# Kernel optimization log

Hardware: AMD Instinct MI355X
Metric: run time of the kernel (lower is better)

The kernel has to match this reference:

```python
import jax, jax.numpy as jnp
import numpy as np

D = 64        # inner_feature_len (dim)
HID = 128     # hidden_channels of the edge MLP
NCONV = 2     # n_conv
STEPS = 3     # Set2Set processing_steps
NSEG = 128    # number of graphs in the batch


def setup_inputs() -> dict:
    key = jax.random.key(0)
    ks = jax.random.split(key, 30)
    N, E, FN, FE = 10000, 64000, 92, 41
    s = 0.05
    p = lambda i, shape: jax.random.normal(ks[i], shape, jnp.float32) * s
    return {
        "x": jax.random.normal(ks[0], (N, FN), jnp.float32),
        "edge_attr": jax.random.uniform(ks[1], (E, FE), dtype=jnp.float32),
        "lin0_w": p(2, (D, FN)), "lin0_b": p(3, (D,)),
        "nn1_w": p(4, (HID, FE)), "nn1_b": p(5, (HID,)),
        "nn2_w": p(6, (D * D, HID)), "nn2_b": p(7, (D * D,)),
        "root_w": p(8, (D, D)), "conv_b": p(9, (D,)),
        "gru_w_ih": p(10, (3 * D, D)), "gru_w_hh": p(11, (3 * D, D)),
        "gru_b_ih": p(12, (3 * D,)), "gru_b_hh": p(13, (3 * D,)),
        "lstm_w_ih": p(14, (4 * D, 2 * D)), "lstm_w_hh": p(15, (4 * D, D)),
        "lstm_b_ih": p(16, (4 * D,)), "lstm_b_hh": p(17, (4 * D,)),
        "lin1_w": p(18, (D, 2 * D)), "lin1_b": p(19, (D,)),
        "lin2_w": p(20, (1, D)), "lin2_b": p(21, (1,)),
        "edge_index": jax.random.randint(ks[22], (2, E), 0, N, dtype=jnp.int32),
        "batch": jnp.sort(jax.random.randint(ks[23], (N,), 0, NSEG, dtype=jnp.int32)),
    }


def _gru_step(m, h, w_ih, w_hh, b_ih, b_hh):
    # torch GRU gate order: r, z, n
    gi = m @ w_ih.T + b_ih
    gh = h @ w_hh.T + b_hh
    r = jax.nn.sigmoid(gi[:, :D] + gh[:, :D])
    z = jax.nn.sigmoid(gi[:, D:2 * D] + gh[:, D:2 * D])
    n = jnp.tanh(gi[:, 2 * D:] + r * gh[:, 2 * D:])
    return (1.0 - z) * n + z * h


def _forward(x, edge_attr, lin0_w, lin0_b, nn1_w, nn1_b, nn2_w, nn2_b, root_w, conv_b,
             gru_w_ih, gru_w_hh, gru_b_ih, gru_b_hh, lstm_w_ih, lstm_w_hh, lstm_b_ih,
             lstm_b_hh, lin1_w, lin1_b, lin2_w, lin2_b, edge_index, batch):
    N = x.shape[0]
    src, dst = edge_index[0], edge_index[1]

    # Edge-conditioned weight matrices: [E, D, D] (dominant intermediate)
    We = (jax.nn.relu(edge_attr @ nn1_w.T + nn1_b) @ nn2_w.T + nn2_b).reshape(-1, D, D)
    deg = jnp.clip(jax.ops.segment_sum(jnp.ones_like(src, jnp.float32), dst, num_segments=N), 1.0, None)

    out = jax.nn.relu(x @ lin0_w.T + lin0_b)   # [N, D]
    h = out                                     # GRU hidden (num_layers=1)
    for _ in range(NCONV):
        # NNConv: gather -> per-edge matmul -> scatter-mean, plus root transform + bias
        msg = jnp.einsum('ei,eio->eo', out[src], We)                 # [E, D]
        agg = jax.ops.segment_sum(msg, dst, num_segments=N) / deg[:, None]
        m = jax.nn.relu(agg + out @ root_w.T + conv_b)
        h = _gru_step(m, h, gru_w_ih, gru_w_hh, gru_b_ih, gru_b_hh)
        out = h

    # Set2Set pooling (LSTM-attention readout)
    q_star = jnp.zeros((NSEG, 2 * D), x.dtype)
    hl = jnp.zeros((NSEG, D), x.dtype)
    cl = jnp.zeros((NSEG, D), x.dtype)
    for _ in range(STEPS):
        g = q_star @ lstm_w_ih.T + lstm_b_ih + hl @ lstm_w_hh.T + lstm_b_hh
        i = jax.nn.sigmoid(g[:, :D])
        f = jax.nn.sigmoid(g[:, D:2 * D])
        gg = jnp.tanh(g[:, 2 * D:3 * D])
        o = jax.nn.sigmoid(g[:, 3 * D:])
        cl = f * cl + i * gg
        hl = o * jnp.tanh(cl)
        q = hl                                   # [NSEG, D]
        e = jnp.sum(out * q[batch], axis=-1)     # [N]
        mmax = jax.ops.segment_max(e, batch, num_segments=NSEG)
        a = jnp.exp(e - mmax[batch])
        denom = jax.ops.segment_sum(a, batch, num_segments=NSEG)
        a = a / denom[batch]
        r = jax.ops.segment_sum(a[:, None] * out, batch, num_segments=NSEG)  # [NSEG, D]
        q_star = jnp.concatenate([q, r], axis=1)

    y = jax.nn.relu(q_star @ lin1_w.T + lin1_b) @ lin2_w.T + lin2_b
    return y.reshape(-1)


def reference(x, edge_attr, lin0_w, lin0_b, nn1_w, nn1_b, nn2_w, nn2_b, root_w, conv_b,
              gru_w_ih, gru_w_hh, gru_b_ih, gru_b_hh, lstm_w_ih, lstm_w_hh, lstm_b_ih,
              lstm_b_hh, lin1_w, lin1_b, lin2_w, lin2_b, edge_index, batch):
    return _forward(x, edge_attr, lin0_w, lin0_b, nn1_w, nn1_b, nn2_w, nn2_b, root_w,
                    conv_b, gru_w_ih, gru_w_hh, gru_b_ih, gru_b_hh, lstm_w_ih, lstm_w_hh,
                    lstm_b_ih, lstm_b_hh, lin1_w, lin1_b, lin2_w, lin2_b, edge_index, batch)
```

## Files before the change

### kernel.cpp

```cpp
#include <hip/hip_runtime.h>
#include <hip/hip_bf16.h>
#include <math.h>

#define DD 64
#define HIDC 128
#define FN 92
#define FE 41
#define S2CAP 192

typedef unsigned short u16;
typedef short bf16x8 __attribute__((ext_vector_type(8)));
typedef float f32x4 __attribute__((ext_vector_type(4)));

__device__ __forceinline__ float sigmoidf_(float x){ return 1.f/(1.f+expf(-x)); }

__device__ __forceinline__ u16 f2bf(float v){
  union { float f; unsigned u; } x; x.f = v;
  unsigned r = x.u + 0x7fff + ((x.u >> 16) & 1);
  return (u16)(r >> 16);
}
__device__ __forceinline__ float bf2f(u16 v){
  union { float f; unsigned u; } x; x.u = ((unsigned)v) << 16;
  return x.f;
}
__device__ __forceinline__ void split_bf(float v, u16& h, u16& l){
  h = f2bf(v); l = f2bf(v - bf2f(h));
}

__global__ void k_pack(const float* __restrict__ lin0_w, const float* __restrict__ nn1_w,
                       const float* __restrict__ root_w, const float* __restrict__ gwih,
                       const float* __restrict__ gwhh, const float* __restrict__ lwih,
                       const float* __restrict__ lwhh, const float* __restrict__ lin1_w,
                       float* __restrict__ lin0T, float* __restrict__ nn1T,
                       float* __restrict__ rootT, float* __restrict__ wihT,
                       float* __restrict__ whhT, float* __restrict__ lwihT,
                       float* __restrict__ lwhhT, float* __restrict__ lin1T)
{
  int idx = blockIdx.x*blockDim.x + threadIdx.x;
  if (idx < 92*64){ int k=idx/64, o=idx%64; lin0T[k*64+o] = lin0_w[o*92+k]; return; } idx -= 92*64;
  if (idx < 41*128){ int k=idx/128, h=idx%128; nn1T[k*128+h] = nn1_w[h*41+k]; return; } idx -= 41*128;
  if (idx < 64*64){ int i=idx/64, o=idx%64; rootT[i*64+o] = root_w[o*64+i]; return; } idx -= 64*64;
  if (idx < 64*192){ int i=idx/192, g=idx%192; wihT[i*192+g] = gwih[g*64+i]; return; } idx -= 64*192;
  if (idx < 64*192){ int i=idx/192, g=idx%192; whhT[i*192+g] = gwhh[g*64+i]; return; } idx -= 64*192;
  if (idx < 128*256){ int j=idx/256, t=idx%256; lwihT[j*256+t] = lwih[t*128+j]; return; } idx -= 128*256;
  if (idx < 64*256){ int j=idx/256, t=idx%256; lwhhT[j*256+t] = lwhh[t*64+j]; return; } idx -= 64*256;
  if (idx < 128*64){ int j=idx/64, t=idx%64; lin1T[j*64+t] = lin1_w[t*128+j]; return; }
}

__global__ void k_pack_b2(const float* __restrict__ nn2_w,
                          u16* __restrict__ BhT, u16* __restrict__ BlT){
  int idx = blockIdx.x*256 + threadIdx.x;
  if (idx >= 524288) return;
  int i  = idx & 63;
  int ho = (idx >> 6) & 4095;
  int c  = idx >> 18;
  int h = ho >> 6, o = ho & 63;
  float v = nn2_w[(size_t)(i*64+o)*128 + c*64 + h];
  u16 hi, lo; split_bf(v, hi, lo);
  BhT[idx] = hi; BlT[idx] = lo;
}

__global__ void k_pack_b1(const float* __restrict__ nn1_w,
                          u16* __restrict__ BT1h, u16* __restrict__ BT1l){
  int idx = blockIdx.x*256 + threadIdx.x;
  if (idx >= 8192) return;
  int h = idx >> 6, k = idx & 63;
  float v = (k < FE) ? nn1_w[(size_t)h*FE + k] : 0.f;
  u16 hi, lo; split_bf(v, hi, lo);
  BT1h[idx] = hi; BT1l[idx] = lo;
}

__global__ void k_split_ea(const float* __restrict__ ea, const int* __restrict__ sortedE,
                           u16* __restrict__ eaH, u16* __restrict__ eaL, int E){
  int idx = blockIdx.x*256 + threadIdx.x;
  if (idx >= E*64) return;
  int ew = idx >> 6, k = idx & 63;
  int e = sortedE[ew];
  float v = (k < FE) ? ea[(size_t)e*FE + k] : 0.f;
  u16 hi, lo; split_bf(v, hi, lo);
  eaH[idx] = hi; eaL[idx] = lo;
}

__global__ __launch_bounds__(256) void k_node_mlp(const float* __restrict__ x,
    const float* __restrict__ lin0T, const float* __restrict__ lin0_b,
    const float* __restrict__ nn2_b,
    float* __restrict__ out, u16* __restrict__ outH, u16* __restrict__ outL,
    float* __restrict__ bterm, int N)
{
  __shared__ float xs[4][FN];
  int base = blockIdx.x*4;
  for (int i=threadIdx.x; i<4*FN; i+=256){
    int n = base + i/FN;
    xs[i/FN][i%FN] = (n<N) ? x[(size_t)n*FN + i%FN] : 0.f;
  }
  __syncthreads();
  int ln = threadIdx.x>>6, o = threadIdx.x&63;
  int n = base+ln;
  if (n>=N) return;
  float acc = lin0_b[o];
  #pragma unroll 4
  for (int k=0;k<FN;k++) acc = fmaf(xs[ln][k], lin0T[k*64+o], acc);
  float v = fmaxf(acc, 0.f);
  out[(size_t)n*64+o] = v;
  u16 hi, lo; split_bf(v, hi, lo);
  outH[(size_t)n*64+o] = hi;
  outL[(size_t)n*64+o] = lo;
  float bt = 0.f;
  #pragma unroll 8
  for (int i=0;i<64;i++) bt = fmaf(__shfl(v, i, 64), nn2_b[i*64+o], bt);
  bterm[(size_t)n*64+o] = bt;
}

__global__ void k_count(const int* __restrict__ dst, const int* __restrict__ src,
                        float* __restrict__ deg, int* __restrict__ scnt, int E){
  int e = blockIdx.x*blockDim.x + threadIdx.x;
  if (e < E){
    atomicAdd(&deg[dst[e]], 1.f);
    atomicAdd(&scnt[src[e]], 1);
  }
}

__global__ void k_scan1(const int* __restrict__ cnt, int* __restrict__ excl,
                        int* __restrict__ bsum, int N){
  __shared__ int buf[256];
  int i = blockIdx.x*256 + threadIdx.x;
  int v = (i<N) ? cnt[i] : 0;
  buf[threadIdx.x] = v;
  __syncthreads();
  #pragma unroll
  for (int off=1; off<256; off<<=1){
    int t = (threadIdx.x>=off) ? buf[threadIdx.x-off] : 0;
    __syncthreads();
    buf[threadIdx.x] += t;
    __syncthreads();
  }
  if (i<N) excl[i] = buf[threadIdx.x] - v;
  if (threadIdx.x==255) bsum[blockIdx.x] = buf[255];
}
__global__ void k_scan2(int* __restrict__ bsum, int nb){
  __shared__ int buf[256];
  int v = (threadIdx.x<nb) ? bsum[threadIdx.x] : 0;
  buf[threadIdx.x] = v;
  __syncthreads();
  #pragma unroll
  for (int off=1; off<256; off<<=1){
    int t = (threadIdx.x>=off) ? buf[threadIdx.x-off] : 0;
    __syncthreads();
    buf[threadIdx.x] += t;
    __syncthreads();
  }
  if (threadIdx.x<nb) bsum[threadIdx.x] = buf[threadIdx.x] - v;
}
__global__ void k_scan3(int* __restrict__ starts, int* __restrict__ cursor,
                        const int* __restrict__ bsum, int N, int E){
  int i = blockIdx.x*256 + threadIdx.x;
  if (i<N){
    int s = starts[i] + bsum[blockIdx.x];
    starts[i] = s;
    cursor[i] = s;
  }
  if (i==0) starts[N] = E;
}

__global__ void k_sort(const int* __restrict__ src, const int* __restrict__ dst,
                       int* __restrict__ cursor, int* __restrict__ sortedE,
                       int* __restrict__ srcS, int* __restrict__ dstS, int E){
  int e = blockIdx.x*256 + threadIdx.x;
  if (e < E){
    int s = src[e];
    int p = atomicAdd(&cursor[s], 1);
    sortedE[p] = e;
    srcS[p] = s;
    dstS[p] = dst[e];
  }
}

__global__ __launch_bounds__(256,3) void k_edge_mlp_mfma(
    const u16* __restrict__ eaH, const u16* __restrict__ eaL,
    const u16* __restrict__ BT1h, const u16* __restrict__ BT1l,
    const float* __restrict__ nn1_b, float* __restrict__ hidden, int E)
{
  __shared__ float st[4][16][68];
  const int wave = threadIdx.x >> 6;
  const int lane = threadIdx.x & 63;
  const int row  = lane & 15;
  const int quad = lane >> 4;
  const int m0 = blockIdx.x*128 + (wave>>1)*64;
  const int n0 = (wave&1)*64;

  bf16x8 AH0[4], AH1[4], AL0[4], AL1[4];
  #pragma unroll
  for (int p=0;p<4;p++){
    int ar = min(m0 + p*16 + row, E-1);
    const u16* aH = eaH + (size_t)ar*64 + quad*8;
    const u16* aL = eaL + (size_t)ar*64 + quad*8;
    AH0[p] = *(const bf16x8*)(aH);
    AH1[p] = *(const bf16x8*)(aH + 32);
    AL0[p] = *(const bf16x8*)(aL);
    AL1[p] = *(const bf16x8*)(aL + 32);
  }
  f32x4 acc[4][4];
  #pragma unroll
  for (int p=0;p<4;p++)
    #pragma unroll
    for (int t=0;t<4;t++) acc[p][t] = (f32x4){0.f,0.f,0.f,0.f};

  #pragma unroll
  for (int t=0;t<4;t++){
    const u16* bH = BT1h + (size_t)(n0 + t*16 + row)*64 + quad*8;
    const u16* bL = BT1l + (size_t)(n0 + t*16 + row)*64 + quad*8;
    bf16x8 bh0 = *(const bf16x8*)(bH);
    bf16x8 bh1 = *(const bf16x8*)(bH + 32);
    bf16x8 bl0 = *(const bf16x8*)(bL);
    bf16x8 bl1 = *(const bf16x8*)(bL + 32);
    #pragma unroll
    for (int p=0;p<4;p++){
      f32x4 a = acc[p][t];
      a = __builtin_amdgcn_mfma_f32_16x16x32_bf16(AH0[p], bh0, a, 0,0,0);
      a = __builtin_amdgcn_mfma_f32_16x16x32_bf16(AH1[p], bh1, a, 0,0,0);
      a = __builtin_amdgcn_mfma_f32_16x16x32_bf16(AH0[p], bl0, a, 0,0,0);
      a = __builtin_amdgcn_mfma_f32_16x16x32_bf16(AH1[p], bl1, a, 0,0,0);
      a = __builtin_amdgcn_mfma_f32_16x16x32_bf16(AL0[p], bh0, a, 0,0,0);
      a = __builtin_amdgcn_mfma_f32_16x16x32_bf16(AL1[p], bh1, a, 0,0,0);
      acc[p][t] = a;
    }
  }

  const int lr = lane >> 4;
  const int lc = (lane & 15) * 4;
  #pragma unroll
  for (int p=0;p<4;p++){
    #pragma unroll
    for (int t=0;t<4;t++){
      float bias = nn1_b[n0 + t*16 + row];
      #pragma unroll
      for (int r=0;r<4;r++) st[wave][quad*4+r][t*16+row] = fmaxf(acc[p][t][r] + bias, 0.f);
    }
    #pragma unroll
    for (int it=0; it<4; it++){
      int mrow = it*4 + lr;
      float4 v;
      v.x = st[wave][mrow][lc+0];
      v.y = st[wave][mrow][lc+1];
      v.z = st[wave][mrow][lc+2];
      v.w = st[wave][mrow][lc+3];
      int m = m0 + p*16 + mrow;
      if (m < E) *(float4*)(hidden + (size_t)m*128 + n0 + lc) = v;
    }
  }
}

__global__ __launch_bounds__(256,3) void k_qgemm_mfma(
    const u16* __restrict__ Ah, const u16* __restrict__ Al,
    const u16* __restrict__ BhT, const u16* __restrict__ BlT,
    float* __restrict__ C, int M)
{
  __shared__ float st[4][16][68];
  const int wave = threadIdx.x >> 6;
  const int lane = threadIdx.x & 63;
  const int row  = lane & 15;
  const int quad = lane >> 4;
  const int m0 = blockIdx.y * 64;
  const int n0 = blockIdx.x * 256 + wave * 64;

  bf16x8 AH0[4], AH1[4], AL0[4], AL1[4];
  #pragma unroll
  for (int p=0;p<4;p++){
    int ar = min(m0 + p*16 + row, M-1);
    const u16* aH = Ah + (size_t)ar*64 + quad*8;
    const u16* aL = Al + (size_t)ar*64 + quad*8;
    AH0[p] = *(const bf16x8*)(aH);
    AH1[p] = *(const bf16x8*)(aH + 32);
    AL0[p] = *(const bf16x8*)(aL);
    AL1[p] = *(const bf16x8*)(aL + 32);
  }
  f32x4 acc[4][4];
  #pragma unroll
  for (int p=0;p<4;p++)
    #pragma unroll
    for (int t=0;t<4;t++) acc[p][t] = (f32x4){0.f,0.f,0.f,0.f};

  #pragma unroll
  for (int t=0;t<4;t++){
    const u16* bH = BhT + (size_t)(n0 + t*16 + row)*64 + quad*8;
    const u16* bL = BlT + (size_t)(n0 + t*16 + row)*64 + quad*8;
    bf16x8 bh0 = *(const bf16x8*)(bH);
    bf16x8 bh1 = *(const bf16x8*)(bH + 32);
    bf16x8 bl0 = *(const bf16x8*)(bL);
    bf16x8 bl1 = *(const bf16x8*)(bL + 32);
    #pragma unroll
    for (int p=0;p<4;p++){
      f32x4 a = acc[p][t];
      a = __builtin_amdgcn_mfma_f32_16x16x32_bf16(AH0[p], bh0, a, 0,0,0);
      a = __builtin_amdgcn_mfma_f32_16x16x32_bf16(AH1[p], bh1, a, 0,0,0);
      a = __builtin_amdgcn_mfma_f32_16x16x32_bf16(AH0[p], bl0, a, 0,0,0);
      a = __builtin_amdgcn_mfma_f32_16x16x32_bf16(AH1[p], bl1, a, 0,0,0);
      a = __builtin_amdgcn_mfma_f32_16x16x32_bf16(AL0[p], bh0, a, 0,0,0);
      a = __builtin_amdgcn_mfma_f32_16x16x32_bf16(AL1[p], bh1, a, 0,0,0);
      acc[p][t] = a;
    }
  }

  const int lr = lane >> 4;
  const int lc = (lane & 15) * 4;
  #pragma unroll
  for (int p=0;p<4;p++){
    #pragma unroll
    for (int t=0;t<4;t++)
      #pragma unroll
      for (int r=0;r<4;r++) st[wave][quad*4+r][t*16+row] = acc[p][t][r];
    #pragma unroll
    for (int it=0; it<4; it++){
      int mrow = it*4 + lr;
      float4 v;
      v.x = st[wave][mrow][lc+0];
      v.y = st[wave][mrow][lc+1];
      v.z = st[wave][mrow][lc+2];
      v.w = st[wave][mrow][lc+3];
      int m = m0 + p*16 + mrow;
      if (m < M) *(float4*)(C + (size_t)m*4096 + n0 + lc) = v;
    }
  }
}

template<int PASS>
__global__ __launch_bounds__(256) void k_edge_gather(const float* __restrict__ Q,
    const float* __restrict__ hidden, int h0,
    const float* __restrict__ bterm, const int* __restrict__ srcS,
    const int* __restrict__ dstS,
    float* __restrict__ msg, float* __restrict__ agg, int E)
{
  __shared__ float hs[4][2][64];
  __shared__ float red[4][2][64];
  const int wv = threadIdx.x>>6, lane = threadIdx.x&63;
  const int ew0 = (blockIdx.x*4 + wv)*2;
  const bool v0 = (ew0 < E), v1 = (ew0+1 < E);
  const int e0 = v0 ? ew0 : 0;
  const int e1 = v1 ? ew0+1 : 0;
  const int s0 = srcS[e0], s1 = srcS[e1];
  hs[wv][0][lane] = hidden[(size_t)e0*128 + h0 + lane];
  hs[wv][1][lane] = hidden[(size_t)e1*128 + h0 + lane];
  const int sg = lane>>4, oq = lane&15;
  const float* q0 = Q + (size_t)s0*4096 + sg*64 + oq*4;
  const float* q1 = Q + (size_t)s1*4096 + sg*64 + oq*4;
  float a00=0.f,a01=0.f,a02=0.f,a03=0.f;
  float a10=0.f,a11=0.f,a12=0.f,a13=0.f;
  #pragma unroll
  for (int j=0;j<16;j++){
    float4 qa = *(const float4*)(q0 + j*256);
    float4 qb = *(const float4*)(q1 + j*256);
    float h0v = hs[wv][0][j*4 + sg];
    float h1v = hs[wv][1][j*4 + sg];
    a00 = fmaf(h0v, qa.x, a00); a01 = fmaf(h0v, qa.y, a01);
    a02 = fmaf(h0v, qa.z, a02); a03 = fmaf(h0v, qa.w, a03);
    a10 = fmaf(h1v, qb.x, a10); a11 = fmaf(h1v, qb.y, a11);
    a12 = fmaf(h1v, qb.z, a12); a13 = fmaf(h1v, qb.w, a13);
  }
  a00 += __shfl_xor(a00,16); a00 += __shfl_xor(a00,32);
  a01 += __shfl_xor(a01,16); a01 += __shfl_xor(a01,32);
  a02 += __shfl_xor(a02,16); a02 += __shfl_xor(a02,32);
  a03 += __shfl_xor(a03,16); a03 += __shfl_xor(a03,32);
  a10 += __shfl_xor(a10,16); a10 += __shfl_xor(a10,32);
  a11 += __shfl_xor(a11,16); a11 += __shfl_xor(a11,32);
  a12 += __shfl_xor(a12,16); a12 += __shfl_xor(a12,32);
  a13 += __shfl_xor(a13,16); a13 += __shfl_xor(a13,32);
  if (lane < 16){
    float4 r0; r0.x=a00; r0.y=a01; r0.z=a02; r0.w=a03;
    float4 r1; r1.x=a10; r1.y=a11; r1.z=a12; r1.w=a13;
    *(float4*)&red[wv][0][lane*4] = r0;
    *(float4*)&red[wv][1][lane*4] = r1;
  }
  if (v0){
    float rv = red[wv][0][lane];
    if (PASS == 0) msg[(size_t)ew0*64 + lane] = bterm[(size_t)s0*64 + lane] + rv;
    else atomicAdd(&agg[(size_t)dstS[ew0]*64 + lane], msg[(size_t)ew0*64 + lane] + rv);
  }
  if (v1){
    float rv = red[wv][1][lane];
    if (PASS == 0) msg[(size_t)(ew0+1)*64 + lane] = bterm[(size_t)s1*64 + lane] + rv;
    else atomicAdd(&agg[(size_t)dstS[ew0+1]*64 + lane], msg[(size_t)(ew0+1)*64 + lane] + rv);
  }
}

__global__ __launch_bounds__(256) void k_node_update(const float* __restrict__ outOld,
    const float* __restrict__ agg, const float* __restrict__ deg,
    const float* __restrict__ rootT, const float* __restrict__ conv_b,
    const float* __restrict__ wihT, const float* __restrict__ whhT,
    const float* __restrict__ b_ih, const float* __restrict__ b_hh,
    const float* __restrict__ nn2_b,
    float* __restrict__ outNew, u16* __restrict__ outH, u16* __restrict__ outL,
    float* __restrict__ bterm, int N)
{
  __shared__ float hs[4][64];
  __shared__ float ms[4][64];
  int ln = threadIdx.x>>6, o = threadIdx.x&63;
  int n = blockIdx.x*4+ln;
  bool ok = (n<N);
  float h = ok ? outOld[(size_t)n*64+o] : 0.f;
  hs[ln][o] = h;
  __syncthreads();
  float root = 0.f;
  #pragma unroll 8
  for (int i=0;i<64;i++) root = fmaf(hs[ln][i], rootT[i*64+o], root);
  float d = ok ? fmaxf(deg[n], 1.f) : 1.f;
  float a = ok ? agg[(size_t)n*64+o]/d : 0.f;
  float m = fmaxf(a + root + conv_b[o], 0.f);
  ms[ln][o] = m;
  __syncthreads();
  float gir=b_ih[o], giz=b_ih[64+o], gin=b_ih[128+o];
  float ghr=b_hh[o], ghz=b_hh[64+o], ghn=b_hh[128+o];
  #pragma unroll 4
  for (int i=0;i<64;i++){
    float mi = ms[ln][i], hi = hs[ln][i];
    gir = fmaf(mi, wihT[i*192+o],      gir);
    giz = fmaf(mi, wihT[i*192+64+o],   giz);
    gin = fmaf(mi, wihT[i*192+128+o],  gin);
    ghr = fmaf(hi, whhT[i*192+o],      ghr);
    ghz = fmaf(hi, whhT[i*192+64+o],   ghz);
    ghn = fmaf(hi, whhT[i*192+128+o],  ghn);
  }
  float r = sigmoidf_(gir+ghr);
  float z = sigmoidf_(giz+ghz);
  float nn = tanhf(gin + r*ghn);
  if (ok){
    float v = (1.f-z)*nn + z*h;
    outNew[(size_t)n*64+o] = v;
    u16 hi16, lo16; split_bf(v, hi16, lo16);
    outH[(size_t)n*64+o] = hi16;
    outL[(size_t)n*64+o] = lo16;
    float bt = 0.f;
    #pragma unroll 8
    for (int i=0;i<64;i++) bt = fmaf(__shfl(v, i, 64), nn2_b[i*64+o], bt);
    bterm[(size_t)n*64+o] = bt;
  }
}

__global__ __launch_bounds__(256) void k_set2set(const float* __restrict__ out,
    const int* __restrict__ batch, int N,
    const float* __restrict__ lwihT, const float* __restrict__ lwhhT,
    const float* __restrict__ b_ih, const float* __restrict__ b_hh,
    const float* __restrict__ lin1T, const float* __restrict__ lin1_b,
    const float* __restrict__ lin2_w, const float* __restrict__ lin2_b,
    float* __restrict__ y)
{
  __shared__ float X[S2CAP][65];
  __shared__ float earr[S2CAP];
  __shared__ float qstar[128], hl[64], cl[64], g[256];
  __shared__ float rpart[4][64], spart[4], redm[4], zs[64];
  __shared__ int sb[2];
  const int tid = threadIdx.x;
  const int b = blockIdx.x;
  const int wid = tid>>6, lane = tid&63;
  if (tid < 128) qstar[tid] = 0.f;
  if (tid < 64){ hl[tid]=0.f; cl[tid]=0.f; }
  if (tid == 0){
    int lo=0, hi=N;
    while (lo<hi){ int mid=(lo+hi)>>1; if (batch[mid] < b) lo=mid+1; else hi=mid; }
    sb[0]=lo;
    int lo2=lo, hi2=N;
    while (lo2<hi2){ int mid=(lo2+hi2)>>1; if (batch[mid] < b+1) lo2=mid+1; else hi2=mid; }
    sb[1]=lo2;
  }
  __syncthreads();
  const int nlo = sb[0], nhi = sb[1], nn = nhi - nlo;
  const bool single = (nn <= S2CAP);
  if (single){
    for (int idx = tid; idx < nn*64; idx += 256){
      X[idx>>6][idx&63] = out[(size_t)(nlo + (idx>>6))*64 + (idx&63)];
    }
  }
  __syncthreads();

  for (int step=0; step<3; step++){
    float gs = b_ih[tid] + b_hh[tid];
    for (int j=0;j<128;j++) gs = fmaf(qstar[j], lwihT[j*256+tid], gs);
    for (int j=0;j<64;j++)  gs = fmaf(hl[j],    lwhhT[j*256+tid], gs);
    g[tid] = gs;
    __syncthreads();
    if (tid < 64){
      float ig = sigmoidf_(g[tid]);
      float fg = sigmoidf_(g[64+tid]);
      float gg = tanhf(g[128+tid]);
      float og = sigmoidf_(g[192+tid]);
      float c = fg*cl[tid] + ig*gg;
      cl[tid] = c;
      hl[tid] = og*tanhf(c);
    }
    __syncthreads();

    if (single){
      float lm = -INFINITY;
      for (int n = tid; n < nn; n += 256){
        float acc = 0.f;
        #pragma unroll 8
        for (int d=0; d<64; d++) acc = fmaf(X[n][d], hl[d], acc);
        earr[n] = acc;
        lm = fmaxf(lm, acc);
      }
      lm = fmaxf(lm, __shfl_xor(lm,1));  lm = fmaxf(lm, __shfl_xor(lm,2));
      lm = fmaxf(lm, __shfl_xor(lm,4));  lm = fmaxf(lm, __shfl_xor(lm,8));
      lm = fmaxf(lm, __shfl_xor(lm,16)); lm = fmaxf(lm, __shfl_xor(lm,32));
      if (lane==0) redm[wid] = lm;
      __syncthreads();
      if (tid==0) redm[0] = fmaxf(fmaxf(redm[0],redm[1]), fmaxf(redm[2],redm[3]));
      __syncthreads();
      const float gmax = redm[0];
      float ls = 0.f;
      for (int n = tid; n < nn; n += 256){
        float a = expf(earr[n] - gmax);
        earr[n] = a;
        ls += a;
      }
      ls += __shfl_xor(ls,1);  ls += __shfl_xor(ls,2);  ls += __shfl_xor(ls,4);
      ls += __shfl_xor(ls,8);  ls += __shfl_xor(ls,16); ls += __shfl_xor(ls,32);
      if (lane==0) spart[wid] = ls;
      __syncthreads();
      float racc = 0.f;
      for (int n = wid; n < nn; n += 4) racc = fmaf(earr[n], X[n][lane], racc);
      rpart[wid][lane] = racc;
      __syncthreads();
      if (tid < 64){
        float r = rpart[0][tid]+rpart[1][tid]+rpart[2][tid]+rpart[3][tid];
        float s = spart[0]+spart[1]+spart[2]+spart[3];
        qstar[tid] = hl[tid];
        qstar[64+tid] = (nn>0) ? r/s : 0.f;
      }
      __syncthreads();
    } else {
      float qv = hl[lane];
      float lm = -INFINITY;
      for (int n = nlo + wid; n < nhi; n += 4){
        float p = out[(size_t)n*64 + lane]*qv;
        p += __shfl_xor(p,1); p += __shfl_xor(p,2); p += __shfl_xor(p,4);
        p += __shfl_xor(p,8); p += __shfl_xor(p,16); p += __shfl_xor(p,32);
        lm = fmaxf(lm, p);
      }
      if (lane==0) redm[wid] = lm;
      __syncthreads();
      if (tid==0) redm[0] = fmaxf(fmaxf(redm[0],redm[1]), fmaxf(redm[2],redm[3]));
      __syncthreads();
      float gmax = redm[0];
      float sw = 0.f, racc = 0.f;
      for (int n = nlo + wid; n < nhi; n += 4){
        float ol = out[(size_t)n*64 + lane];
        float p = ol*qv;
        p += __shfl_xor(p,1); p += __shfl_xor(p,2); p += __shfl_xor(p,4);
        p += __shfl_xor(p,8); p += __shfl_xor(p,16); p += __shfl_xor(p,32);
        float a = expf(p - gmax);
        sw += a;
        racc = fmaf(a, ol, racc);
      }
      rpart[wid][lane] = racc;
      if (lane==0) spart[wid] = sw;
      __syncthreads();
      if (tid < 64){
        float r = rpart[0][tid]+rpart[1][tid]+rpart[2][tid]+rpart[3][tid];
        float s = spart[0]+spart[1]+spart[2]+spart[3];
        qstar[tid] = hl[tid];
        qstar[64+tid] = (nn>0) ? r/s : 0.f;
      }
      __syncthreads();
    }
  }
  if (tid < 64){
    float acc = lin1_b[tid];
    for (int j=0;j<128;j++) acc = fmaf(qstar[j], lin1T[j*64+tid], acc);
    zs[tid] = fmaxf(acc, 0.f);
  }
  __syncthreads();
  if (tid < 64){
    float v = zs[lane]*lin2_w[lane];
    v += __shfl_xor(v,1); v += __shfl_xor(v,2); v += __shfl_xor(v,4);
    v += __shfl_xor(v,8); v += __shfl_xor(v,16); v += __shfl_xor(v,32);
    if (lane==0) y[b] = v + lin2_b[0];
  }
}

extern "C" void kernel_launch(void* const* d_in, const int* in_sizes, int n_in,
                              void* d_out, int out_size, void* d_ws, size_t ws_size,
                              hipStream_t stream)
{
  const float* x      = (const float*)d_in[0];
  const float* eattr  = (const float*)d_in[1];
  const float* lin0_w = (const float*)d_in[2];
  const float* lin0_b = (const float*)d_in[3];
  const float* nn1_w  = (const float*)d_in[4];
  const float* nn1_b  = (const float*)d_in[5];
  const float* nn2_w  = (const float*)d_in[6];
  const float* nn2_b  = (const float*)d_in[7];
  const float* root_w = (const float*)d_in[8];
  const float* conv_b = (const float*)d_in[9];
  const float* gwih   = (const float*)d_in[10];
  const float* gwhh   = (const float*)d_in[11];
  const float* gbih   = (const float*)d_in[12];
  const float* gbhh   = (const float*)d_in[13];
  const float* lwih   = (const float*)d_in[14];
  const float* lwhh   = (const float*)d_in[15];
  const float* lbih   = (const float*)d_in[16];
  const float* lbhh   = (const float*)d_in[17];
  const float* lin1_w = (const float*)d_in[18];
  const float* lin1_b = (const float*)d_in[19];
  const float* lin2_w = (const float*)d_in[20];
  const float* lin2_b = (const float*)d_in[21];
  const int*   eidx   = (const int*)d_in[22];
  const int*   batch  = (const int*)d_in[23];

  const int N = in_sizes[0]/FN;
  const int E = in_sizes[1]/FE;
  const int* srcI = eidx;
  const int* dstI = eidx + E;

  char* w = (char*)d_ws;
  size_t off = 0;
  auto alloc = [&](size_t bytes)->char* {
    char* p = w + off;
    off = (off + bytes + 255) & ~(size_t)255;
    return p;
  };
  float* degw  = (float*)alloc((size_t)N*4);
  int*   scnt  = (int*)alloc((size_t)N*4);
  int*   starts= (int*)alloc((size_t)(N+1)*4);
  int*   cursor= (int*)alloc((size_t)N*4);
  int*   bsum  = (int*)alloc((size_t)256*4);
  int*   sortedE=(int*)alloc((size_t)E*4);
  int*   srcS  = (int*)alloc((size_t)E*4);
  int*   dstS  = (int*)alloc((size_t)E*4);
  float* outA  = (float*)alloc((size_t)N*64*4);
  float* outB  = (float*)alloc((size_t)N*64*4);
  u16*   outAH = (u16*)alloc((size_t)N*64*2);
  u16*   outAL = (u16*)alloc((size_t)N*64*2);
  u16*   outBH = (u16*)alloc((size_t)N*64*2);
  u16*   outBL = (u16*)alloc((size_t)N*64*2);
  float* agg   = (float*)alloc((size_t)N*64*4);
  float* bterm = (float*)alloc((size_t)N*64*4);
  float* hidden= (float*)alloc((size_t)E*128*4);
  float* msg   = (float*)alloc((size_t)E*64*4);
  u16*   B2hT  = (u16*)alloc((size_t)524288*2);
  u16*   B2lT  = (u16*)alloc((size_t)524288*2);
  u16*   BT1h  = (u16*)alloc((size_t)8192*2);
  u16*   BT1l  = (u16*)alloc((size_t)8192*2);
  float* lin0T = (float*)alloc((size_t)92*64*4);
  float* nn1T  = (float*)alloc((size_t)41*128*4);
  float* rootT = (float*)alloc((size_t)64*64*4);
  float* wihT  = (float*)alloc((size_t)64*192*4);
  float* whhT  = (float*)alloc((size_t)64*192*4);
  float* lwihT = (float*)alloc((size_t)128*256*4);
  float* lwhhT = (float*)alloc((size_t)64*256*4);
  float* lin1T = (float*)alloc((size_t)128*64*4);
  float* Q     = (float*)alloc((size_t)N*4096*4);
  u16* eaH = (u16*)Q;
  u16* eaL = eaH + (size_t)E*64;

  const int NB = (N+255)/256;

  hipMemsetAsync(degw, 0, (size_t)N*4, stream);
  hipMemsetAsync(scnt, 0, (size_t)N*4, stream);
  k_pack<<<(97152+255)/256, 256, 0, stream>>>(lin0_w, nn1_w, root_w, gwih, gwhh,
      lwih, lwhh, lin1_w, lin0T, nn1T, rootT, wihT, whhT, lwihT, lwhhT, lin1T);
  k_pack_b2<<<524288/256, 256, 0, stream>>>(nn2_w, B2hT, B2lT);
  k_pack_b1<<<8192/256, 256, 0, stream>>>(nn1_w, BT1h, BT1l);
  k_node_mlp<<<(N+3)/4, 256, 0, stream>>>(x, lin0T, lin0_b, nn2_b, outA, outAH, outAL, bterm, N);
  k_count<<<(E+255)/256, 256, 0, stream>>>(dstI, srcI, degw, scnt, E);
  k_scan1<<<NB, 256, 0, stream>>>(scnt, starts, bsum, N);
  k_scan2<<<1, 256, 0, stream>>>(bsum, NB);
  k_scan3<<<NB, 256, 0, stream>>>(starts, cursor, bsum, N, E);
  k_sort<<<(E+255)/256, 256, 0, stream>>>(srcI, dstI, cursor, sortedE, srcS, dstS, E);
  k_split_ea<<<((size_t)E*64+255)/256, 256, 0, stream>>>(eattr, sortedE, eaH, eaL, E);
  k_edge_mlp_mfma<<<(E+127)/128, 256, 0, stream>>>(eaH, eaL, BT1h, BT1l, nn1_b, hidden, E);

  float* cur = outA; float* nxt = outB;
  u16* curH = outAH; u16* curL = outAL;
  u16* nxtH = outBH; u16* nxtL = outBL;
  const dim3 qgrid(16, (N+63)/64);
  const int gatherGx = (E+7)/8;
  for (int conv=0; conv<2; conv++){
    hipMemsetAsync(agg, 0, (size_t)N*64*4, stream);
    k_qgemm_mfma<<<qgrid, 256, 0, stream>>>(curH, curL, B2hT, B2lT, Q, N);
    k_edge_gather<0><<<gatherGx, 256, 0, stream>>>(Q, hidden, 0, bterm, srcS, dstS, msg, agg, E);
    k_qgemm_mfma<<<qgrid, 256, 0, stream>>>(curH, curL, B2hT + 262144, B2lT + 262144, Q, N);
    k_edge_gather<1><<<gatherGx, 256, 0, stream>>>(Q, hidden, 64, bterm, srcS, dstS, msg, agg, E);
    k_node_update<<<(N+3)/4, 256, 0, stream>>>(cur, agg, degw, rootT, conv_b,
        wihT, whhT, gbih, gbhh, nn2_b, nxt, nxtH, nxtL, bterm, N);
    float* t = cur; cur = nxt; nxt = t;
    u16* th = curH; curH = nxtH; nxtH = th;
    u16* tl = curL; curL = nxtL; nxtL = tl;
  }

  k_set2set<<<128, 256, 0, stream>>>(cur, batch, N, lwihT, lwhhT, lbih, lbhh,
      lin1T, lin1_b, lin2_w, lin2_b, (float*)d_out);
}
```

Measured before the change: 667.0 us.

## Swap MFMA operand order to store directly, and process four edges per wave in gather

The two MFMA GEMM kernels now pass the B tile as the first operand and the A tile as the second. Each lane then holds four consecutive output columns of one row, so results can be written as float4 straight to global memory. This drops the shared-memory staging buffer and the full accumulator array, which should cut LDS traffic and register pressure. Separately, the edge gather kernel handles four edges per wave instead of two, with the grid halved to match, to raise memory-level parallelism on the Q row loads at the cost of more registers.

```diff
diff --git a/kernel.cpp b/kernel.cpp
--- a/kernel.cpp
+++ b/kernel.cpp
@@ -180,9 +180,8 @@
     const u16* __restrict__ BT1h, const u16* __restrict__ BT1l,
     const float* __restrict__ nn1_b, float* __restrict__ hidden, int E)
 {
-  __shared__ float st[4][16][68];
+  const int lane = threadIdx.x & 63;
   const int wave = threadIdx.x >> 6;
-  const int lane = threadIdx.x & 63;
   const int row  = lane & 15;
   const int quad = lane >> 4;
   const int m0 = blockIdx.x*128 + (wave>>1)*64;
@@ -199,53 +198,36 @@
     AL0[p] = *(const bf16x8*)(aL);
     AL1[p] = *(const bf16x8*)(aL + 32);
   }
-  f32x4 acc[4][4];
-  #pragma unroll
-  for (int p=0;p<4;p++)
-    #pragma unroll
-    for (int t=0;t<4;t++) acc[p][t] = (f32x4){0.f,0.f,0.f,0.f};
-
-  #pragma unroll
-  for (int t=0;t<4;t++){
-    const u16* bH = BT1h + (size_t)(n0 + t*16 + row)*64 + quad*8;
-    const u16* bL = BT1l + (size_t)(n0 + t*16 + row)*64 + quad*8;
+  #pragma unroll
+  for (int tb=0;tb<4;tb++){
+    const u16* bH = BT1h + (size_t)(n0 + tb*16 + row)*64 + quad*8;
+    const u16* bL = BT1l + (size_t)(n0 + tb*16 + row)*64 + quad*8;
     bf16x8 bh0 = *(const bf16x8*)(bH);
     bf16x8 bh1 = *(const bf16x8*)(bH + 32);
     bf16x8 bl0 = *(const bf16x8*)(bL);
     bf16x8 bl1 = *(const bf16x8*)(bL + 32);
+    float4 bias;
+    {
+      int nb = n0 + tb*16 + quad*4;
+      bias.x = nn1_b[nb+0]; bias.y = nn1_b[nb+1];
+      bias.z = nn1_b[nb+2]; bias.w = nn1_b[nb+3];
+    }
     #pragma unroll
-    for (int p=0;p<4;p++){
-      f32x4 a = acc[p][t];
-      a = __builtin_amdgcn_mfma_f32_16x16x32_bf16(AH0[p], bh0, a, 0,0,0);
-      a = __builtin_amdgcn_mfma_f32_16x16x32_bf16(AH1[p], bh1, a, 0,0,0);
-      a = __builtin_amdgcn_mfma_f32_16x16x32_bf16(AH0[p], bl0, a, 0,0,0);
-      a = __builtin_amdgcn_mfma_f32_16x16x32_bf16(AH1[p], bl1, a, 0,0,0);
-      a = __builtin_amdgcn_mfma_f32_16x16x32_bf16(AL0[p], bh0, a, 0,0,0);
-      a = __builtin_amdgcn_mfma_f32_16x16x32_bf16(AL1[p], bh1, a, 0,0,0);
-      acc[p][t] = a;
-    }
-  }
-
-  const int lr = lane >> 4;
-  const int lc = (lane & 15) * 4;
-  #pragma unroll
-  for (int p=0;p<4;p++){
-    #pragma unroll
-    for (int t=0;t<4;t++){
-      float bias = nn1_b[n0 + t*16 + row];
-      #pragma unroll
-      for (int r=0;r<4;r++) st[wave][quad*4+r][t*16+row] = fmaxf(acc[p][t][r] + bias, 0.f);
-    }
-    #pragma unroll
-    for (int it=0; it<4; it++){
-      int mrow = it*4 + lr;
-      float4 v;
-      v.x = st[wave][mrow][lc+0];
-      v.y = st[wave][mrow][lc+1];
-      v.z = st[wave][mrow][lc+2];
-      v.w = st[wave][mrow][lc+3];
-      int m = m0 + p*16 + mrow;
-      if (m < E) *(float4*)(hidden + (size_t)m*128 + n0 + lc) = v;
+    for (int ta=0;ta<4;ta++){
+      f32x4 a = {0.f,0.f,0.f,0.f};
+      a = __builtin_amdgcn_mfma_f32_16x16x32_bf16(bh0, AH0[ta], a, 0,0,0);
+      a = __builtin_amdgcn_mfma_f32_16x16x32_bf16(bh1, AH1[ta], a, 0,0,0);
+      a = __builtin_amdgcn_mfma_f32_16x16x32_bf16(bl0, AH0[ta], a, 0,0,0);
+      a = __builtin_amdgcn_mfma_f32_16x16x32_bf16(bl1, AH1[ta], a, 0,0,0);
+      a = __builtin_amdgcn_mfma_f32_16x16x32_bf16(bh0, AL0[ta], a, 0,0,0);
+      a = __builtin_amdgcn_mfma_f32_16x16x32_bf16(bh1, AL1[ta], a, 0,0,0);
+      int m = m0 + ta*16 + row;
+      if (m < E){
+        float4 v;
+        v.x = fmaxf(a[0]+bias.x, 0.f); v.y = fmaxf(a[1]+bias.y, 0.f);
+        v.z = fmaxf(a[2]+bias.z, 0.f); v.w = fmaxf(a[3]+bias.w, 0.f);
+        *(float4*)(hidden + (size_t)m*128 + n0 + tb*16 + quad*4) = v;
+      }
     }
   }
 }
@@ -255,9 +237,8 @@
     const u16* __restrict__ BhT, const u16* __restrict__ BlT,
     float* __restrict__ C, int M)
 {
-  __shared__ float st[4][16][68];
+  const int lane = threadIdx.x & 63;
   const int wave = threadIdx.x >> 6;
-  const int lane = threadIdx.x & 63;
   const int row  = lane & 15;
   const int quad = lane >> 4;
   const int m0 = blockIdx.y * 64;
@@ -274,51 +255,29 @@
     AL0[p] = *(const bf16x8*)(aL);
     AL1[p] = *(const bf16x8*)(aL + 32);
   }
-  f32x4 acc[4][4];
-  #pragma unroll
-  for (int p=0;p<4;p++)
-    #pragma unroll
-    for (int t=0;t<4;t++) acc[p][t] = (f32x4){0.f,0.f,0.f,0.f};
-
-  #pragma unroll
-  for (int t=0;t<4;t++){
-    const u16* bH = BhT + (size_t)(n0 + t*16 + row)*64 + quad*8;
-    const u16* bL = BlT + (size_t)(n0 + t*16 + row)*64 + quad*8;
+
+  #pragma unroll
+  for (int tb=0;tb<4;tb++){
+    const u16* bH = BhT + (size_t)(n0 + tb*16 + row)*64 + quad*8;
+    const u16* bL = BlT + (size_t)(n0 + tb*16 + row)*64 + quad*8;
     bf16x8 bh0 = *(const bf16x8*)(bH);
     bf16x8 bh1 = *(const bf16x8*)(bH + 32);
     bf16x8 bl0 = *(const bf16x8*)(bL);
     bf16x8 bl1 = *(const bf16x8*)(bL + 32);
     #pragma unroll
-    for (int p=0;p<4;p++){
-      f32x4 a = acc[p][t];
-      a = __builtin_amdgcn_mfma_f32_16x16x32_bf16(AH0[p], bh0, a, 0,0,0);
-      a = __builtin_amdgcn_mfma_f32_16x16x32_bf16(AH1[p], bh1, a, 0,0,0);
-      a = __builtin_amdgcn_mfma_f32_16x16x32_bf16(AH0[p], bl0, a, 0,0,0);
-      a = __builtin_amdgcn_mfma_f32_16x16x32_bf16(AH1[p], bl1, a, 0,0,0);
-      a = __builtin_amdgcn_mfma_f32_16x16x32_bf16(AL0[p], bh0, a, 0,0,0);
-      a = __builtin_amdgcn_mfma_f32_16x16x32_bf16(AL1[p], bh1, a, 0,0,0);
-      acc[p][t] = a;
-    }
-  }
-
-  const int lr = lane >> 4;
-  const int lc = (lane & 15) * 4;
-  #pragma unroll
-  for (int p=0;p<4;p++){
-    #pragma unroll
-    for (int t=0;t<4;t++)
-      #pragma unroll
-      for (int r=0;r<4;r++) st[wave][quad*4+r][t*16+row] = acc[p][t][r];
-    #pragma unroll
-    for (int it=0; it<4; it++){
-      int mrow = it*4 + lr;
-      float4 v;
-      v.x = st[wave][mrow][lc+0];
-      v.y = st[wave][mrow][lc+1];
-      v.z = st[wave][mrow][lc+2];
-      v.w = st[wave][mrow][lc+3];
-      int m = m0 + p*16 + mrow;
-      if (m < M) *(float4*)(C + (size_t)m*4096 + n0 + lc) = v;
+    for (int ta=0;ta<4;ta++){
+      f32x4 a = {0.f,0.f,0.f,0.f};
+      a = __builtin_amdgcn_mfma_f32_16x16x32_bf16(bh0, AH0[ta], a, 0,0,0);
+      a = __builtin_amdgcn_mfma_f32_16x16x32_bf16(bh1, AH1[ta], a, 0,0,0);
+      a = __builtin_amdgcn_mfma_f32_16x16x32_bf16(bl0, AH0[ta], a, 0,0,0);
+      a = __builtin_amdgcn_mfma_f32_16x16x32_bf16(bl1, AH1[ta], a, 0,0,0);
+      a = __builtin_amdgcn_mfma_f32_16x16x32_bf16(bh0, AL0[ta], a, 0,0,0);
+      a = __builtin_amdgcn_mfma_f32_16x16x32_bf16(bh1, AL1[ta], a, 0,0,0);
+      int m = m0 + ta*16 + row;
+      if (m < M){
+        float4 v; v.x=a[0]; v.y=a[1]; v.z=a[2]; v.w=a[3];
+        *(float4*)(C + (size_t)m*4096 + n0 + tb*16 + quad*4) = v;
+      }
     }
   }
 }
@@ -330,55 +289,62 @@
     const int* __restrict__ dstS,
     float* __restrict__ msg, float* __restrict__ agg, int E)
 {
-  __shared__ float hs[4][2][64];
-  __shared__ float red[4][2][64];
+  __shared__ float hs[4][4][64];
+  __shared__ float red[4][4][64];
   const int wv = threadIdx.x>>6, lane = threadIdx.x&63;
-  const int ew0 = (blockIdx.x*4 + wv)*2;
-  const bool v0 = (ew0 < E), v1 = (ew0+1 < E);
-  const int e0 = v0 ? ew0 : 0;
-  const int e1 = v1 ? ew0+1 : 0;
-  const int s0 = srcS[e0], s1 = srcS[e1];
-  hs[wv][0][lane] = hidden[(size_t)e0*128 + h0 + lane];
-  hs[wv][1][lane] = hidden[(size_t)e1*128 + h0 + lane];
+  const int ewb = (blockIdx.x*4 + wv)*4;
+  int ee[4]; bool vv[4]; int ss[4];
+  #pragma unroll
+  for (int i=0;i<4;i++){
+    vv[i] = (ewb+i < E);
+    ee[i] = vv[i] ? ewb+i : 0;
+    ss[i] = srcS[ee[i]];
+    hs[wv][i][lane] = hidden[(size_t)ee[i]*128 + h0 + lane];
+  }
   const int sg = lane>>4, oq = lane&15;
-  const float* q0 = Q + (size_t)s0*4096 + sg*64 + oq*4;
-  const float* q1 = Q + (size_t)s1*4096 + sg*64 + oq*4;
-  float a00=0.f,a01=0.f,a02=0.f,a03=0.f;
-  float a10=0.f,a11=0.f,a12=0.f,a13=0.f;
+  float acc[4][4];
+  #pragma unroll
+  for (int i=0;i<4;i++)
+    #pragma unroll
+    for (int r=0;r<4;r++) acc[i][r] = 0.f;
+  const float* qp[4];
+  #pragma unroll
+  for (int i=0;i<4;i++) qp[i] = Q + (size_t)ss[i]*4096 + sg*64 + oq*4;
   #pragma unroll
   for (int j=0;j<16;j++){
-    float4 qa = *(const float4*)(q0 + j*256);
-    float4 qb = *(const float4*)(q1 + j*256);
-    float h0v = hs[wv][0][j*4 + sg];
-    float h1v = hs[wv][1][j*4 + sg];
-    a00 = fmaf(h0v, qa.x, a00); a01 = fmaf(h0v, qa.y, a01);
-    a02 = fmaf(h0v, qa.z, a02); a03 = fmaf(h0v, qa.w, a03);
-    a10 = fmaf(h1v, qb.x, a10); a11 = fmaf(h1v, qb.y, a11);
-    a12 = fmaf(h1v, qb.z, a12); a13 = fmaf(h1v, qb.w, a13);
-  }
-  a00 += __shfl_xor(a00,16); a00 += __shfl_xor(a00,32);
-  a01 += __shfl_xor(a01,16); a01 += __shfl_xor(a01,32);
-  a02 += __shfl_xor(a02,16); a02 += __shfl_xor(a02,32);
-  a03 += __shfl_xor(a03,16); a03 += __shfl_xor(a03,32);
-  a10 += __shfl_xor(a10,16); a10 += __shfl_xor(a10,32);
-  a11 += __shfl_xor(a11,16); a11 += __shfl_xor(a11,32);
-  a12 += __shfl_xor(a12,16); a12 += __shfl_xor(a12,32);
-  a13 += __shfl_xor(a13,16); a13 += __shfl_xor(a13,32);
+    #pragma unroll
+    for (int i=0;i<4;i++){
+      float4 q = *(const float4*)(qp[i] + j*256);
+      float hv = hs[wv][i][j*4 + sg];
+      acc[i][0] = fmaf(hv, q.x, acc[i][0]);
+      acc[i][1] = fmaf(hv, q.y, acc[i][1]);
+      acc[i][2] = fmaf(hv, q.z, acc[i][2]);
+      acc[i][3] = fmaf(hv, q.w, acc[i][3]);
+    }
+  }
+  #pragma unroll
+  for (int i=0;i<4;i++){
+    #pragma unroll
+    for (int r=0;r<4;r++){
+      acc[i][r] += __shfl_xor(acc[i][r],16);
+      acc[i][r] += __shfl_xor(acc[i][r],32);
+    }
+  }
   if (lane < 16){
-    float4 r0; r0.x=a00; r0.y=a01; r0.z=a02; r0.w=a03;
-    float4 r1; r1.x=a10; r1.y=a11; r1.z=a12; r1.w=a13;
-    *(float4*)&red[wv][0][lane*4] = r0;
-    *(float4*)&red[wv][1][lane*4] = r1;
-  }
-  if (v0){
-    float rv = red[wv][0][lane];
-    if (PASS == 0) msg[(size_t)ew0*64 + lane] = bterm[(size_t)s0*64 + lane] + rv;
-    else atomicAdd(&agg[(size_t)dstS[ew0]*64 + lane], msg[(size_t)ew0*64 + lane] + rv);
-  }
-  if (v1){
-    float rv = red[wv][1][lane];
-    if (PASS == 0) msg[(size_t)(ew0+1)*64 + lane] = bterm[(size_t)s1*64 + lane] + rv;
-    else atomicAdd(&agg[(size_t)dstS[ew0+1]*64 + lane], msg[(size_t)(ew0+1)*64 + lane] + rv);
+    #pragma unroll
+    for (int i=0;i<4;i++){
+      float4 r0; r0.x=acc[i][0]; r0.y=acc[i][1]; r0.z=acc[i][2]; r0.w=acc[i][3];
+      *(float4*)&red[wv][i][lane*4] = r0;
+    }
+  }
+  #pragma unroll
+  for (int i=0;i<4;i++){
+    if (vv[i]){
+      float rv = red[wv][i][lane];
+      int ew = ewb+i;
+      if (PASS == 0) msg[(size_t)ew*64 + lane] = bterm[(size_t)ss[i]*64 + lane] + rv;
+      else atomicAdd(&agg[(size_t)dstS[ew]*64 + lane], msg[(size_t)ew*64 + lane] + rv);
+    }
   }
 }
 
@@ -672,7 +638,7 @@
   u16* curH = outAH; u16* curL = outAL;
   u16* nxtH = outBH; u16* nxtL = outBL;
   const dim3 qgrid(16, (N+63)/64);
-  const int gatherGx = (E+7)/8;
+  const int gatherGx = (E+15)/16;
   for (int conv=0; conv<2; conv++){
     hipMemsetAsync(agg, 0, (size_t)N*64*4, stream);
     k_qgemm_mfma<<<qgrid, 256, 0, stream>>>(curH, curL, B2hT, B2lT, Q, N);
```

Measured after the change: 719.7 us. 7.9% more time.
